# Kernel optimization log

Hardware: AMD Instinct MI355X
Metric: run time of the kernel (lower is better)

## Reference

```python
import jax, jax.numpy as jnp
import numpy as np

D = 1024
H = 16
HD = D // H


def setup_inputs() -> dict:
    key = jax.random.key(0)
    ks = jax.random.split(key, 11)
    B, S = 4, 1024
    s = 0.02
    return {
        "q": jax.random.normal(ks[0], (B, S, D), jnp.float32),
        "k": jax.random.normal(ks[1], (B, S, D), jnp.float32),
        "v": jax.random.normal(ks[2], (B, S, D), jnp.float32),
        "Wq": jax.random.normal(ks[3], (D, D), jnp.float32) * s,
        "bq": jnp.zeros((D,), jnp.float32),
        "Wk": jax.random.normal(ks[4], (D, D), jnp.float32) * s,
        "bk": jnp.zeros((D,), jnp.float32),
        "Wv": jax.random.normal(ks[5], (D, D), jnp.float32) * s,
        "bv": jnp.zeros((D,), jnp.float32),
        "Wo": jax.random.normal(ks[6], (D, D), jnp.float32) * s,
        "bo": jnp.zeros((D,), jnp.float32),
    }


def _split_heads(x):
    # [B, S, D] -> [B, H, S, HD]
    B, S, _ = x.shape
    return x.reshape(B, S, H, HD).transpose(0, 2, 1, 3)


def reference(q, k, v, Wq, bq, Wk, bk, Wv, bv, Wo, bo):
    # Projections followed by ReLU (faithful to the original module)
    qh = _split_heads(jax.nn.relu(q @ Wq + bq))
    kh = _split_heads(jax.nn.relu(k @ Wk + bk))
    vh = _split_heads(jax.nn.relu(v @ Wv + bv))
    # NOTE: original scales by sqrt(input_dim), not sqrt(head_dim)
    scale = 1.0 / jnp.sqrt(jnp.float32(D))
    scores = jnp.einsum("bhsd,bhtd->bhst", qh, kh) * scale  # [B,H,S,S]
    weights = jax.nn.softmax(scores, axis=-1)  # dropout is identity in eval
    attn = jnp.einsum("bhst,bhtd->bhsd", weights, vh)  # [B,H,S,HD]
    B, _, S, _ = attn.shape
    attn = attn.transpose(0, 2, 1, 3).reshape(B, S, D)
    return attn @ Wo + bo
```

## Files before the change

### kernel.cpp

```cpp
#include <hip/hip_runtime.h>
#include <math.h>

#define Dm 1024
#define Hn 16
#define HDn 64
#define Sn 1024

typedef __attribute__((ext_vector_type(8))) __bf16 bf16x8;
typedef __attribute__((ext_vector_type(4))) float floatx4;

__device__ __forceinline__ void async_ld16(void* lds, const void* g) {
    __builtin_amdgcn_global_load_lds(
        (const __attribute__((address_space(1))) void*)g,
        (__attribute__((address_space(3))) void*)lds,
        16, 0, 0);
}

struct PrepArgs {
    const float* qkv[3];
    __bf16*      qkv_o[3];
    const float* W[4];
    __bf16*      WT[4];
    float*       out_zero;
};

__global__ __launch_bounds__(256) void prep_kernel(PrepArgs a)
{
    __shared__ float sT[64][65];
    const int z = blockIdx.z, x = blockIdx.x, tid = threadIdx.x;

    if (z < 3) {
        const float* src = a.qkv[z];
        __bf16* dst = a.qkv_o[z];
        const int lin = x * 256 + tid;
        const float4 v0 = ((const float4*)src)[lin * 2];
        const float4 v1 = ((const float4*)src)[lin * 2 + 1];
        bf16x8 o;
        o[0] = (__bf16)v0.x; o[1] = (__bf16)v0.y; o[2] = (__bf16)v0.z; o[3] = (__bf16)v0.w;
        o[4] = (__bf16)v1.x; o[5] = (__bf16)v1.y; o[6] = (__bf16)v1.z; o[7] = (__bf16)v1.w;
        ((bf16x8*)dst)[lin] = o;
    } else if (z < 7) {
        if (x >= 256) return;
        const float* W = a.W[z - 3];
        __bf16* O = a.WT[z - 3];
        const int bi = (x >> 4) * 64, bj = (x & 15) * 64;
        const int colr = tid & 63, rowg = tid >> 6;
        #pragma unroll
        for (int i = 0; i < 16; ++i) {
            const int kk = i * 4 + rowg;
            sT[kk][colr] = W[(size_t)(bi + kk) * Dm + bj + colr];
        }
        __syncthreads();
        #pragma unroll
        for (int i = 0; i < 16; ++i) {
            const int rn = i * 4 + rowg;
            O[(size_t)(bj + rn) * Dm + bi + colr] = (__bf16)sT[colr][rn];
        }
    } else {
        float4* o = (float4*)a.out_zero;
        const int i = (x * 256 + tid) * 2;
        const float4 zz = make_float4(0.f, 0.f, 0.f, 0.f);
        o[i] = zz;
        o[i + 1] = zz;
    }
}

struct GemmArgs {
    const __bf16* X[3];
    const __bf16* WT[3];
    const float*  bias[3];
    void*         out[3];
    int   layout[3];
    float esc[3];
};

__global__ __launch_bounds__(256) void gemm_bf16_kernel(GemmArgs args)
{
    __shared__ __align__(16) __bf16 sA[128 * 32];
    __shared__ __align__(16) __bf16 sB[128 * 32];

    const int z = blockIdx.z;
    const __bf16* __restrict__ Xb  = args.X[z];
    const __bf16* __restrict__ WTb = args.WT[z];
    const float*  __restrict__ bias = args.bias[z];
    void* __restrict__ outp = args.out[z];
    const int layout = args.layout[z];
    const float escale = args.esc[z];

    const int tid = threadIdx.x;
    const int id = blockIdx.x + (blockIdx.y << 3);
    const int bm = (((id & 7) << 2) | (id >> 6)) * 128;
    const int bn = ((id >> 3) & 7) * 128;

    const int lane = tid & 63;
    const int wave = tid >> 6;
    const int wm = (wave & 1) * 64;
    const int wn = (wave >> 1) * 64;
    const int l15 = lane & 15, quad = lane >> 4;

    floatx4 acc[4][4];
    #pragma unroll
    for (int mi = 0; mi < 4; ++mi)
        #pragma unroll
        for (int ni = 0; ni < 4; ++ni)
            acc[mi][ni] = (floatx4){0.f, 0.f, 0.f, 0.f};

    const int c0 = tid,       r0 = c0 >> 2, q0 = (c0 & 3) ^ (r0 & 3);
    const int c1 = tid + 256, r1 = c1 >> 2, q1 = (c1 & 3) ^ (r1 & 3);
    const __bf16* gA0 = Xb  + (size_t)(bm + r0) * Dm + q0 * 8;
    const __bf16* gA1 = Xb  + (size_t)(bm + r1) * Dm + q1 * 8;
    const __bf16* gB0 = WTb + (size_t)(bn + r0) * Dm + q0 * 8;
    const __bf16* gB1 = WTb + (size_t)(bn + r1) * Dm + q1 * 8;
    char* lA0 = (char*)sA + (tid & 192) * 16;
    char* lA1 = (char*)sA + (256 + (tid & 192)) * 16;
    char* lB0 = (char*)sB + (tid & 192) * 16;
    char* lB1 = (char*)sB + (256 + (tid & 192)) * 16;

    const __bf16* fA[4];
    const __bf16* fB[4];
    #pragma unroll
    for (int mi = 0; mi < 4; ++mi) {
        const int r = wm + mi * 16 + l15;
        fA[mi] = sA + r * 32 + ((quad ^ (r & 3)) * 8);
    }
    #pragma unroll
    for (int ni = 0; ni < 4; ++ni) {
        const int r = wn + ni * 16 + l15;
        fB[ni] = sB + r * 32 + ((quad ^ (r & 3)) * 8);
    }

    for (int kt = 0; kt < Dm; kt += 32) {
        async_ld16(lA0, gA0 + kt);
        async_ld16(lA1, gA1 + kt);
        async_ld16(lB0, gB0 + kt);
        async_ld16(lB1, gB1 + kt);
        __syncthreads();

        bf16x8 af[4], bfr[4];
        #pragma unroll
        for (int mi = 0; mi < 4; ++mi) af[mi] = *(const bf16x8*)fA[mi];
        #pragma unroll
        for (int ni = 0; ni < 4; ++ni) bfr[ni] = *(const bf16x8*)fB[ni];
        #pragma unroll
        for (int mi = 0; mi < 4; ++mi)
            #pragma unroll
            for (int ni = 0; ni < 4; ++ni)
                acc[mi][ni] = __builtin_amdgcn_mfma_f32_16x16x32_bf16(
                    af[mi], bfr[ni], acc[mi][ni], 0, 0, 0);
        __syncthreads();
    }

    #pragma unroll
    for (int mi = 0; mi < 4; ++mi) {
        #pragma unroll
        for (int ni = 0; ni < 4; ++ni) {
            const int n = bn + wn + ni * 16 + l15;
            const float bv = bias[n];
            const int h = n >> 6, d = n & 63;
            #pragma unroll
            for (int reg = 0; reg < 4; ++reg) {
                const int m = bm + wm + mi * 16 + quad * 4 + reg;
                const int b = m >> 10, s = m & 1023;
                float v = fmaxf(acc[mi][ni][reg] + bv, 0.0f) * escale;
                if (layout == 0)
                    ((__bf16*)outp)[((size_t)(b * Hn + h) * 1024 + s) * 64 + d] = (__bf16)v;
                else
                    ((__bf16*)outp)[((size_t)(b * Hn + h) * 64 + d) * 1024 + s] = (__bf16)v;
            }
        }
    }
}

__global__ __launch_bounds__(256) void gemm_splitk_kernel(
    const __bf16* __restrict__ Xb, const __bf16* __restrict__ WTb,
    const float* __restrict__ bias, float* __restrict__ outp)
{
    __shared__ __align__(16) __bf16 sA[128 * 32];
    __shared__ __align__(16) __bf16 sB[128 * 32];

    const int tid = threadIdx.x;
    const int kz = blockIdx.z;
    const int id = blockIdx.x + (blockIdx.y << 3);
    const int bm = (((id & 7) << 2) | (id >> 6)) * 128;
    const int bn = ((id >> 3) & 7) * 128;

    const int lane = tid & 63;
    const int wave = tid >> 6;
    const int wm = (wave & 1) * 64;
    const int wn = (wave >> 1) * 64;
    const int l15 = lane & 15, quad = lane >> 4;

    floatx4 acc[4][4];
    #pragma unroll
    for (int mi = 0; mi < 4; ++mi)
        #pragma unroll
        for (int ni = 0; ni < 4; ++ni)
            acc[mi][ni] = (floatx4){0.f, 0.f, 0.f, 0.f};

    const int c0 = tid,       r0 = c0 >> 2, q0 = (c0 & 3) ^ (r0 & 3);
    const int c1 = tid + 256, r1 = c1 >> 2, q1 = (c1 & 3) ^ (r1 & 3);
    const int kofs = kz * 512;
    const __bf16* gA0 = Xb  + (size_t)(bm + r0) * Dm + kofs + q0 * 8;
    const __bf16* gA1 = Xb  + (size_t)(bm + r1) * Dm + kofs + q1 * 8;
    const __bf16* gB0 = WTb + (size_t)(bn + r0) * Dm + kofs + q0 * 8;
    const __bf16* gB1 = WTb + (size_t)(bn + r1) * Dm + kofs + q1 * 8;
    char* lA0 = (char*)sA + (tid & 192) * 16;
    char* lA1 = (char*)sA + (256 + (tid & 192)) * 16;
    char* lB0 = (char*)sB + (tid & 192) * 16;
    char* lB1 = (char*)sB + (256 + (tid & 192)) * 16;

    const __bf16* fA[4];
    const __bf16* fB[4];
    #pragma unroll
    for (int mi = 0; mi < 4; ++mi) {
        const int r = wm + mi * 16 + l15;
        fA[mi] = sA + r * 32 + ((quad ^ (r & 3)) * 8);
    }
    #pragma unroll
    for (int ni = 0; ni < 4; ++ni) {
        const int r = wn + ni * 16 + l15;
        fB[ni] = sB + r * 32 + ((quad ^ (r & 3)) * 8);
    }

    for (int kt = 0; kt < 512; kt += 32) {
        async_ld16(lA0, gA0 + kt);
        async_ld16(lA1, gA1 + kt);
        async_ld16(lB0, gB0 + kt);
        async_ld16(lB1, gB1 + kt);
        __syncthreads();

        bf16x8 af[4], bfr[4];
        #pragma unroll
        for (int mi = 0; mi < 4; ++mi) af[mi] = *(const bf16x8*)fA[mi];
        #pragma unroll
        for (int ni = 0; ni < 4; ++ni) bfr[ni] = *(const bf16x8*)fB[ni];
        #pragma unroll
        for (int mi = 0; mi < 4; ++mi)
            #pragma unroll
            for (int ni = 0; ni < 4; ++ni)
                acc[mi][ni] = __builtin_amdgcn_mfma_f32_16x16x32_bf16(
                    af[mi], bfr[ni], acc[mi][ni], 0, 0, 0);
        __syncthreads();
    }

    #pragma unroll
    for (int mi = 0; mi < 4; ++mi) {
        #pragma unroll
        for (int ni = 0; ni < 4; ++ni) {
            const int n = bn + wn + ni * 16 + l15;
            const float bv = (kz == 0) ? bias[n] : 0.0f;
            #pragma unroll
            for (int reg = 0; reg < 4; ++reg) {
                const int m = bm + wm + mi * 16 + quad * 4 + reg;
                atomicAdd(outp + (size_t)m * 1024 + n, acc[mi][ni][reg] + bv);
            }
        }
    }
}

__global__ __launch_bounds__(256, 2) void flash_attn_kernel(
    const __bf16* __restrict__ Qh,
    const __bf16* __restrict__ Kh,
    const __bf16* __restrict__ Vt,
    __bf16* __restrict__ ctx)
{
    __shared__ __align__(16) char sKV[2][16384];
    __shared__ __align__(16) __bf16 sP[4][32 * 64];

    const int tid = threadIdx.x;
    const int wave = tid >> 6, lane = tid & 63;
    const int l15 = lane & 15, quad = lane >> 4;

    const int id = blockIdx.x + (blockIdx.y << 3) + (blockIdx.z << 7);
    const int kk = id >> 3;
    const int bh = ((id & 7) << 3) | (kk & 7);
    const int b = bh >> 4, h = bh & 15;
    const int qb = (kk >> 3) * 128 + wave * 32;

    bf16x8 aQ[2][2];
    #pragma unroll
    for (int mi = 0; mi < 2; ++mi)
        #pragma unroll
        for (int ks = 0; ks < 2; ++ks)
            aQ[mi][ks] = *(const bf16x8*)(Qh +
                (size_t)(bh * Sn + qb + mi * 16 + l15) * 64 + ks * 32 + quad * 8);

    const int s0 = tid, s1 = tid + 256;
    const int r0 = s0 >> 3, q0c = (s0 & 7) ^ (r0 & 7);
    const int r1 = s1 >> 3, q1c = (s1 & 7) ^ (r1 & 7);
    const __bf16* gK0 = Kh + (size_t)(bh * Sn + r0) * 64 + q0c * 8;
    const __bf16* gK1 = Kh + (size_t)(bh * Sn + r1) * 64 + q1c * 8;
    const __bf16* gV0 = Vt + (size_t)(bh * 64 + r0) * Sn + q0c * 8;
    const __bf16* gV1 = Vt + (size_t)(bh * 64 + r1) * Sn + q1c * 8;
    const int wofs = (tid & 192) * 16;

    floatx4 oacc[2][4];
    #pragma unroll
    for (int mi = 0; mi < 2; ++mi)
        #pragma unroll
        for (int nf = 0; nf < 4; ++nf)
            oacc[mi][nf] = (floatx4){0.f, 0.f, 0.f, 0.f};
    float lsum[2][4];
    #pragma unroll
    for (int mi = 0; mi < 2; ++mi)
        #pragma unroll
        for (int r = 0; r < 4; ++r) lsum[mi][r] = 0.0f;

    __bf16* sPw = sP[wave];

    {
        char* bK = sKV[0];
        char* bV = sKV[0] + 8192;
        async_ld16(bK + wofs,        gK0);
        async_ld16(bK + 4096 + wofs, gK1);
        async_ld16(bV + wofs,        gV0);
        async_ld16(bV + 4096 + wofs, gV1);
    }

    int cur = 0;
    for (int it = 0; it < 16; ++it) {
        __syncthreads();

        if (it + 1 < 16) {
            const int t0n = (it + 1) * 64;
            char* bK = sKV[cur ^ 1];
            char* bV = sKV[cur ^ 1] + 8192;
            async_ld16(bK + wofs,        gK0 + (size_t)t0n * 64);
            async_ld16(bK + 4096 + wofs, gK1 + (size_t)t0n * 64);
            async_ld16(bV + wofs,        gV0 + t0n);
            async_ld16(bV + 4096 + wofs, gV1 + t0n);
        }

        const __bf16* sK = (const __bf16*)sKV[cur];
        const __bf16* sV = (const __bf16*)(sKV[cur] + 8192);

        floatx4 sc[2][4];
        #pragma unroll
        for (int mi = 0; mi < 2; ++mi)
            #pragma unroll
            for (int nf = 0; nf < 4; ++nf)
                sc[mi][nf] = (floatx4){0.f, 0.f, 0.f, 0.f};
        #pragma unroll
        for (int ks = 0; ks < 2; ++ks) {
            bf16x8 bK[4];
            #pragma unroll
            for (int nf = 0; nf < 4; ++nf) {
                const int n = nf * 16 + l15;
                bK[nf] = *(const bf16x8*)(sK + (n * 8 + (((ks << 2) + quad) ^ (n & 7))) * 8);
            }
            #pragma unroll
            for (int mi = 0; mi < 2; ++mi)
                #pragma unroll
                for (int nf = 0; nf < 4; ++nf)
                    sc[mi][nf] = __builtin_amdgcn_mfma_f32_16x16x32_bf16(
                        aQ[mi][ks], bK[nf], sc[mi][nf], 0, 0, 0);
        }

        #pragma unroll
        for (int mi = 0; mi < 2; ++mi)
            #pragma unroll
            for (int nf = 0; nf < 4; ++nf) {
                const int t = nf * 16 + l15;
                #pragma unroll
                for (int r = 0; r < 4; ++r) {
                    const float p = __builtin_amdgcn_exp2f(fminf(sc[mi][nf][r], 126.0f));
                    const __bf16 pb = (__bf16)p;
                    lsum[mi][r] += (float)pb;
                    const int rr = mi * 16 + quad * 4 + r;
                    sPw[(rr * 8 + ((t >> 3) ^ (rr & 7))) * 8 + (t & 7)] = pb;
                }
            }

        #pragma unroll
        for (int ks = 0; ks < 2; ++ks) {
            bf16x8 aP[2], bV[4];
            #pragma unroll
            for (int mi = 0; mi < 2; ++mi) {
                const int r = mi * 16 + l15;
                aP[mi] = *(const bf16x8*)(sPw + (r * 8 + (((ks << 2) + quad) ^ (r & 7))) * 8);
            }
            #pragma unroll
            for (int nf = 0; nf < 4; ++nf) {
                const int n = nf * 16 + l15;
                bV[nf] = *(const bf16x8*)(sV + (n * 8 + (((ks << 2) + quad) ^ (n & 7))) * 8);
            }
            #pragma unroll
            for (int mi = 0; mi < 2; ++mi)
                #pragma unroll
                for (int nf = 0; nf < 4; ++nf)
                    oacc[mi][nf] = __builtin_amdgcn_mfma_f32_16x16x32_bf16(
                        aP[mi], bV[nf], oacc[mi][nf], 0, 0, 0);
        }

        cur ^= 1;
    }

    float linv[2][4];
    #pragma unroll
    for (int mi = 0; mi < 2; ++mi)
        #pragma unroll
        for (int r = 0; r < 4; ++r) {
            float l = lsum[mi][r];
            l += __shfl_xor(l, 1, 64);
            l += __shfl_xor(l, 2, 64);
            l += __shfl_xor(l, 4, 64);
            l += __shfl_xor(l, 8, 64);
            linv[mi][r] = 1.0f / l;
        }

    #pragma unroll
    for (int mi = 0; mi < 2; ++mi)
        #pragma unroll
        for (int nf = 0; nf < 4; ++nf) {
            const int d = h * 64 + nf * 16 + l15;
            #pragma unroll
            for (int reg = 0; reg < 4; ++reg) {
                const int s = qb + mi * 16 + quad * 4 + reg;
                ctx[(size_t)(b * Sn + s) * Dm + d] =
                    (__bf16)(oacc[mi][nf][reg] * linv[mi][reg]);
            }
        }
}

extern "C" void kernel_launch(void* const* d_in, const int* in_sizes, int n_in,
                              void* d_out, int out_size, void* d_ws, size_t ws_size,
                              hipStream_t stream)
{
    const float* q  = (const float*)d_in[0];
    const float* k  = (const float*)d_in[1];
    const float* v  = (const float*)d_in[2];
    const float* Wq = (const float*)d_in[3];
    const float* bq = (const float*)d_in[4];
    const float* Wk = (const float*)d_in[5];
    const float* bk = (const float*)d_in[6];
    const float* Wv = (const float*)d_in[7];
    const float* bv = (const float*)d_in[8];
    const float* Wo = (const float*)d_in[9];
    const float* bo = (const float*)d_in[10];

    char* ws = (char*)d_ws;
    const size_t MB = 1024 * 1024;
    __bf16* qb_ = (__bf16*)(ws);
    __bf16* kb_ = (__bf16*)(ws + 8 * MB);
    __bf16* vb_ = (__bf16*)(ws + 16 * MB);
    __bf16* WTq = (__bf16*)(ws + 24 * MB);
    __bf16* WTk = (__bf16*)(ws + 26 * MB);
    __bf16* WTv = (__bf16*)(ws + 28 * MB);
    __bf16* WTo = (__bf16*)(ws + 30 * MB);
    __bf16* Qh  = (__bf16*)(ws + 32 * MB);
    __bf16* Kh  = (__bf16*)(ws + 40 * MB);
    __bf16* Vt  = (__bf16*)(ws + 48 * MB);
    __bf16* ctx = (__bf16*)(ws + 56 * MB);

    PrepArgs pa;
    pa.qkv[0] = q; pa.qkv[1] = k; pa.qkv[2] = v;
    pa.qkv_o[0] = qb_; pa.qkv_o[1] = kb_; pa.qkv_o[2] = vb_;
    pa.W[0] = Wq; pa.W[1] = Wk; pa.W[2] = Wv; pa.W[3] = Wo;
    pa.WT[0] = WTq; pa.WT[1] = WTk; pa.WT[2] = WTv; pa.WT[3] = WTo;
    pa.out_zero = (float*)d_out;
    prep_kernel<<<dim3(2048, 1, 8), 256, 0, stream>>>(pa);

    const float QSCALE = 0.0450842200f;

    GemmArgs qkv;
    qkv.X[0] = qb_;  qkv.X[1] = kb_;  qkv.X[2] = vb_;
    qkv.WT[0] = WTq; qkv.WT[1] = WTk; qkv.WT[2] = WTv;
    qkv.bias[0] = bq; qkv.bias[1] = bk; qkv.bias[2] = bv;
    qkv.out[0] = Qh;  qkv.out[1] = Kh;  qkv.out[2] = Vt;
    qkv.layout[0] = 0; qkv.layout[1] = 0; qkv.layout[2] = 1;
    qkv.esc[0] = QSCALE; qkv.esc[1] = 1.0f; qkv.esc[2] = 1.0f;
    gemm_bf16_kernel<<<dim3(8, 32, 3), 256, 0, stream>>>(qkv);

    flash_attn_kernel<<<dim3(8, 16, 4), 256, 0, stream>>>(Qh, Kh, Vt, ctx);

    gemm_splitk_kernel<<<dim3(8, 32, 2), 256, 0, stream>>>(
        ctx, WTo, bo, (float*)d_out);
}
```

Baseline: 226.5 us.

## Double-buffer LDS tiles in projection and split-K GEMMs to overlap loads with MFMA

Both bf16 GEMM kernels now use two LDS buffers per operand. The async global-to-LDS load for the next K tile is issued before the MFMAs on the current tile, with a single barrier per tile. This is meant to hide global load latency behind matrix compute instead of stalling on every tile. It doubles LDS use per block to 32 KB, which may reduce occupancy, and it relies on the barrier placement being enough to avoid overwriting a buffer that is still being read.

```diff
diff --git a/kernel.cpp b/kernel.cpp
--- a/kernel.cpp
+++ b/kernel.cpp
@@ -76,8 +76,8 @@
 
 __global__ __launch_bounds__(256) void gemm_bf16_kernel(GemmArgs args)
 {
-    __shared__ __align__(16) __bf16 sA[128 * 32];
-    __shared__ __align__(16) __bf16 sB[128 * 32];
+    __shared__ __align__(16) __bf16 sA[2][128 * 32];
+    __shared__ __align__(16) __bf16 sB[2][128 * 32];
 
     const int z = blockIdx.z;
     const __bf16* __restrict__ Xb  = args.X[z];
@@ -111,42 +111,53 @@
     const __bf16* gA1 = Xb  + (size_t)(bm + r1) * Dm + q1 * 8;
     const __bf16* gB0 = WTb + (size_t)(bn + r0) * Dm + q0 * 8;
     const __bf16* gB1 = WTb + (size_t)(bn + r1) * Dm + q1 * 8;
-    char* lA0 = (char*)sA + (tid & 192) * 16;
-    char* lA1 = (char*)sA + (256 + (tid & 192)) * 16;
-    char* lB0 = (char*)sB + (tid & 192) * 16;
-    char* lB1 = (char*)sB + (256 + (tid & 192)) * 16;
-
-    const __bf16* fA[4];
-    const __bf16* fB[4];
+    char* const lA = (char*)(&sA[0][0]) + (tid & 192) * 16;
+    char* const lB = (char*)(&sB[0][0]) + (tid & 192) * 16;
+
+    int offA[4], offB[4];
     #pragma unroll
     for (int mi = 0; mi < 4; ++mi) {
         const int r = wm + mi * 16 + l15;
-        fA[mi] = sA + r * 32 + ((quad ^ (r & 3)) * 8);
+        offA[mi] = r * 32 + ((quad ^ (r & 3)) * 8);
     }
     #pragma unroll
     for (int ni = 0; ni < 4; ++ni) {
         const int r = wn + ni * 16 + l15;
-        fB[ni] = sB + r * 32 + ((quad ^ (r & 3)) * 8);
-    }
-
-    for (int kt = 0; kt < Dm; kt += 32) {
-        async_ld16(lA0, gA0 + kt);
-        async_ld16(lA1, gA1 + kt);
-        async_ld16(lB0, gB0 + kt);
-        async_ld16(lB1, gB1 + kt);
-        __syncthreads();
-
+        offB[ni] = r * 32 + ((quad ^ (r & 3)) * 8);
+    }
+
+    auto STAGE = [&](int buf, int kt) {
+        char* a = lA + buf * 8192;
+        char* b = lB + buf * 8192;
+        async_ld16(a,        gA0 + kt);
+        async_ld16(a + 4096, gA1 + kt);
+        async_ld16(b,        gB0 + kt);
+        async_ld16(b + 4096, gB1 + kt);
+    };
+    auto COMPUTE = [&](int buf) {
+        const __bf16* A = &sA[buf][0];
+        const __bf16* B = &sB[buf][0];
         bf16x8 af[4], bfr[4];
         #pragma unroll
-        for (int mi = 0; mi < 4; ++mi) af[mi] = *(const bf16x8*)fA[mi];
-        #pragma unroll
-        for (int ni = 0; ni < 4; ++ni) bfr[ni] = *(const bf16x8*)fB[ni];
+        for (int mi = 0; mi < 4; ++mi) af[mi] = *(const bf16x8*)(A + offA[mi]);
+        #pragma unroll
+        for (int ni = 0; ni < 4; ++ni) bfr[ni] = *(const bf16x8*)(B + offB[ni]);
         #pragma unroll
         for (int mi = 0; mi < 4; ++mi)
             #pragma unroll
             for (int ni = 0; ni < 4; ++ni)
                 acc[mi][ni] = __builtin_amdgcn_mfma_f32_16x16x32_bf16(
                     af[mi], bfr[ni], acc[mi][ni], 0, 0, 0);
+    };
+
+    STAGE(0, 0);
+    __syncthreads();
+    for (int kt = 0; kt < Dm; kt += 64) {
+        STAGE(1, kt + 32);
+        COMPUTE(0);
+        __syncthreads();
+        if (kt + 64 < Dm) STAGE(0, kt + 64);
+        COMPUTE(1);
         __syncthreads();
     }
 
@@ -175,8 +186,8 @@
     const __bf16* __restrict__ Xb, const __bf16* __restrict__ WTb,
     const float* __restrict__ bias, float* __restrict__ outp)
 {
-    __shared__ __align__(16) __bf16 sA[128 * 32];
-    __shared__ __align__(16) __bf16 sB[128 * 32];
+    __shared__ __align__(16) __bf16 sA[2][128 * 32];
+    __shared__ __align__(16) __bf16 sB[2][128 * 32];
 
     const int tid = threadIdx.x;
     const int kz = blockIdx.z;
@@ -204,42 +215,53 @@
     const __bf16* gA1 = Xb  + (size_t)(bm + r1) * Dm + kofs + q1 * 8;
     const __bf16* gB0 = WTb + (size_t)(bn + r0) * Dm + kofs + q0 * 8;
     const __bf16* gB1 = WTb + (size_t)(bn + r1) * Dm + kofs + q1 * 8;
-    char* lA0 = (char*)sA + (tid & 192) * 16;
-    char* lA1 = (char*)sA + (256 + (tid & 192)) * 16;
-    char* lB0 = (char*)sB + (tid & 192) * 16;
-    char* lB1 = (char*)sB + (256 + (tid & 192)) * 16;
-
-    const __bf16* fA[4];
-    const __bf16* fB[4];
+    char* const lA = (char*)(&sA[0][0]) + (tid & 192) * 16;
+    char* const lB = (char*)(&sB[0][0]) + (tid & 192) * 16;
+
+    int offA[4], offB[4];
     #pragma unroll
     for (int mi = 0; mi < 4; ++mi) {
         const int r = wm + mi * 16 + l15;
-        fA[mi] = sA + r * 32 + ((quad ^ (r & 3)) * 8);
+        offA[mi] = r * 32 + ((quad ^ (r & 3)) * 8);
     }
     #pragma unroll
     for (int ni = 0; ni < 4; ++ni) {
         const int r = wn + ni * 16 + l15;
-        fB[ni] = sB + r * 32 + ((quad ^ (r & 3)) * 8);
-    }
-
-    for (int kt = 0; kt < 512; kt += 32) {
-        async_ld16(lA0, gA0 + kt);
-        async_ld16(lA1, gA1 + kt);
-        async_ld16(lB0, gB0 + kt);
-        async_ld16(lB1, gB1 + kt);
-        __syncthreads();
-
+        offB[ni] = r * 32 + ((quad ^ (r & 3)) * 8);
+    }
+
+    auto STAGE = [&](int buf, int kt) {
+        char* a = lA + buf * 8192;
+        char* b = lB + buf * 8192;
+        async_ld16(a,        gA0 + kt);
+        async_ld16(a + 4096, gA1 + kt);
+        async_ld16(b,        gB0 + kt);
+        async_ld16(b + 4096, gB1 + kt);
+    };
+    auto COMPUTE = [&](int buf) {
+        const __bf16* A = &sA[buf][0];
+        const __bf16* B = &sB[buf][0];
         bf16x8 af[4], bfr[4];
         #pragma unroll
-        for (int mi = 0; mi < 4; ++mi) af[mi] = *(const bf16x8*)fA[mi];
-        #pragma unroll
-        for (int ni = 0; ni < 4; ++ni) bfr[ni] = *(const bf16x8*)fB[ni];
+        for (int mi = 0; mi < 4; ++mi) af[mi] = *(const bf16x8*)(A + offA[mi]);
+        #pragma unroll
+        for (int ni = 0; ni < 4; ++ni) bfr[ni] = *(const bf16x8*)(B + offB[ni]);
         #pragma unroll
         for (int mi = 0; mi < 4; ++mi)
             #pragma unroll
             for (int ni = 0; ni < 4; ++ni)
                 acc[mi][ni] = __builtin_amdgcn_mfma_f32_16x16x32_bf16(
                     af[mi], bfr[ni], acc[mi][ni], 0, 0, 0);
+    };
+
+    STAGE(0, 0);
+    __syncthreads();
+    for (int kt = 0; kt < 512; kt += 64) {
+        STAGE(1, kt + 32);
+        COMPUTE(0);
+        __syncthreads();
+        if (kt + 64 < 512) STAGE(0, kt + 64);
+        COMPUTE(1);
         __syncthreads();
     }
 
```

Result: slower. 249.1 us (+9.9%).
